# Optimization experiments

Hardware: AMD Instinct MI355X
Metric: run time of the kernel (lower is better)

## Reference

```python
import jax, jax.numpy as jnp
import numpy as np

FEAT_DIM = 128
GUIDE_DIM = 128
HIDDEN = [1024, 512, 256, 128]
OUT_DIM = 2


def make_coord(shape):
    # grid-center coords in (-1, 1), matching the torch make_coord
    seqs = [(-1.0 + 1.0 / n) + (2.0 / n) * jnp.arange(n, dtype=jnp.float32) for n in shape]
    yy, xx = jnp.meshgrid(seqs[0], seqs[1], indexing='ij')
    return jnp.stack([yy, xx], axis=-1)  # [h, w, 2]


def grid_sample_nearest(img, coord):
    # img: [B, C, H, W]; coord: [B, N, 2] with coord[...,0] along H, coord[...,1] along W
    # replicates F.grid_sample(img, coord.flip(-1)..., mode='nearest', align_corners=False,
    # padding_mode='zeros') followed by permute -> [B, N, C]
    B, C, H, W = img.shape
    iy = jnp.round(((coord[..., 0] + 1.0) * H - 1.0) * 0.5)
    ix = jnp.round(((coord[..., 1] + 1.0) * W - 1.0) * 0.5)
    valid = (iy >= 0) & (iy < H) & (ix >= 0) & (ix < W)
    iyc = jnp.clip(iy, 0, H - 1).astype(jnp.int32)
    ixc = jnp.clip(ix, 0, W - 1).astype(jnp.int32)
    g = jax.vmap(lambda im, y, x: im[:, y, x])(img, iyc, ixc)  # [B, C, N]
    g = g * valid[:, None, :].astype(img.dtype)  # zero padding outside
    return jnp.transpose(g, (0, 2, 1))  # [B, N, C]


def mlp(x, params):
    for W, b in params[:-1]:
        x = jax.nn.relu(x @ W + b)
    W, b = params[-1]
    return x @ W + b


def setup_inputs() -> dict:
    key = jax.random.key(0)
    ks = jax.random.split(key, 16)
    B, h, w = 4, 64, 64
    H_hr = W_hr = 256
    N = H_hr * W_hr  # 65536 query points
    feat = jax.random.normal(ks[0], (B, FEAT_DIM, h, w), jnp.float32)
    coord = jax.random.uniform(ks[1], (B, N, 2), jnp.float32, minval=-1.0, maxval=1.0)
    hr_guide = jax.random.normal(ks[2], (B, GUIDE_DIM, H_hr, W_hr), jnp.float32)
    lr_guide = jax.random.normal(ks[3], (B, GUIDE_DIM, h, w), jnp.float32)
    in_dim = FEAT_DIM + 2 * GUIDE_DIM + 2  # 386
    dims = [in_dim] + HIDDEN + [OUT_DIM]
    inp = {"feat": feat, "coord": coord, "hr_guide": hr_guide, "lr_guide": lr_guide}
    for i in range(len(dims) - 1):
        scale = 1.0 / np.sqrt(dims[i]).astype(np.float32)
        inp[f"W{i}"] = jax.random.normal(ks[4 + 2 * i], (dims[i], dims[i + 1]), jnp.float32) * scale
        inp[f"b{i}"] = jnp.zeros((dims[i + 1],), jnp.float32)
    return inp


def reference(feat, coord, hr_guide, lr_guide, W0, b0, W1, b1, W2, b2, W3, b3, W4, b4):
    params = [(W0, b0), (W1, b1), (W2, b2), (W3, b3), (W4, b4)]
    B, C, h, w = feat.shape
    N = coord.shape[1]
    fc = make_coord((h, w))  # [h, w, 2]
    feat_coord = jnp.broadcast_to(jnp.transpose(fc, (2, 0, 1))[None], (B, 2, h, w))
    q_guide_hr = grid_sample_nearest(hr_guide, coord)  # [B, N, G]
    rx = 1.0 / h
    ry = 1.0 / w
    hw = jnp.array([h, w], dtype=coord.dtype)
    preds = []
    for vx in (-1.0, 1.0):
        for vy in (-1.0, 1.0):
            shift = jnp.array([vx * rx, vy * ry], dtype=coord.dtype)
            coord_ = coord + shift
            q_feat = grid_sample_nearest(feat, coord_)        # [B, N, C]
            q_coord = grid_sample_nearest(feat_coord, coord_)  # [B, N, 2]
            rel_coord = (coord - q_coord) * hw                 # [B, N, 2]
            q_guide_lr = grid_sample_nearest(lr_guide, coord_)  # [B, N, G]
            inp = jnp.concatenate([q_feat, q_guide_hr, q_guide_hr - q_guide_lr, rel_coord], axis=-1)
            pred = mlp(inp.reshape(B * N, -1), params).reshape(B, N, OUT_DIM)
            preds.append(pred)
    preds = jnp.stack(preds, axis=-1)  # [B, N, 2, 4]
    weight = jax.nn.softmax(preds[:, :, 1, :], axis=-1)  # [B, N, 4]
    ret = jnp.sum(preds[:, :, 0, :] * weight, axis=-1, keepdims=True)  # [B, N, 1]
    return ret
```

## Files before the change

kernel.cpp:

```cpp
#include <hip/hip_runtime.h>
#include <cstdint>
#include <cstddef>


typedef unsigned short u16;
typedef unsigned int u32;
typedef _Float16 half8 __attribute__((ext_vector_type(8)));
typedef float floatx4 __attribute__((ext_vector_type(4)));
typedef u32 u32x2 __attribute__((ext_vector_type(2)));
typedef u32 u32x4 __attribute__((ext_vector_type(4)));

__device__ __forceinline__ u16 f2h(float x) {
    _Float16 h = (_Float16)x;
    return __builtin_bit_cast(unsigned short, h);
}
__device__ __forceinline__ float h2f(u16 u) {
    return (float)__builtin_bit_cast(_Float16, u);
}

__device__ __forceinline__ void cp_async16(const void* gsrc, void* lds) {
#if defined(__has_builtin) && __has_builtin(__builtin_amdgcn_global_load_lds)
    __builtin_amdgcn_global_load_lds(
        (__attribute__((address_space(1))) void*)(uintptr_t)gsrc,
        (__attribute__((address_space(3))) void*)(uint32_t)(uintptr_t)lds,
        16, 0, 0);
#else
    *(u32x4*)lds = *(const u32x4*)gsrc;
#endif
}

__global__ void transpose_chw_hwc(const float* __restrict__ src,
                                  u16* __restrict__ dst, int HW) {
    __shared__ float t[32][33];
    const int b = blockIdx.z;
    const int hw0 = blockIdx.x * 32, c0 = blockIdx.y * 32;
    const float* s = src + (size_t)b * 128 * HW;
    u16* d = dst + (size_t)b * HW * 128;
    const int tx = threadIdx.x, ty = threadIdx.y;
#pragma unroll
    for (int j = 0; j < 4; ++j)
        t[ty + j * 8][tx] = s[(size_t)(c0 + ty + j * 8) * HW + hw0 + tx];
    __syncthreads();
#pragma unroll
    for (int j = 0; j < 4; ++j)
        d[(size_t)(hw0 + ty + j * 8) * 128 + c0 + tx] = f2h(t[tx][ty + j * 8]);
}

__global__ void prep_wt(const float* __restrict__ W, u16* __restrict__ Wt,
                        int K, int N, int perm) {
    int idx = blockIdx.x * 256 + threadIdx.x;
    if (idx >= N * K) return;
    int nn = idx / K, kk = idx - nn * K;
    int ka = kk;
    if (perm) {
        int s = kk & 63;
        ka = (kk & ~63) + ((s & 3) << 4) + (s >> 2);
    }
    Wt[idx] = f2h(W[(size_t)ka * N + nn]);
}

__global__ __launch_bounds__(256) void gather_build(
    const float* __restrict__ coord, const u16* __restrict__ hrT,
    const u16* __restrict__ featT, const u16* __restrict__ lrT,
    u16* __restrict__ X, float* __restrict__ rel, int p0) {
    const int wid = threadIdx.x >> 6, lane = threadIdx.x & 63;
    const int pl = blockIdx.x * 4 + wid;
    const int p = p0 + pl;
    const int b = p >> 16;
    const float cy = coord[(size_t)p * 2];
    const float cx = coord[(size_t)p * 2 + 1];
    const u32* hr32 = (const u32*)hrT;
    const u32* ft32 = (const u32*)featT;
    const u32* lr32 = (const u32*)lrT;

    float fy = rintf(((cy + 1.0f) * 256.0f - 1.0f) * 0.5f);
    float fx = rintf(((cx + 1.0f) * 256.0f - 1.0f) * 0.5f);
    bool vh = (fy >= 0.0f) && (fy < 256.0f) && (fx >= 0.0f) && (fx < 256.0f);
    int iy = (int)fminf(fmaxf(fy, 0.0f), 255.0f);
    int ix = (int)fminf(fmaxf(fx, 0.0f), 255.0f);
    u32 hrv = hr32[((((size_t)b * 256 + iy) * 256 + ix) * 128 >> 1) + lane];
    if (!vh) hrv = 0u;
    const float hr_lo = h2f((u16)(hrv & 0xffffu));
    const float hr_hi = h2f((u16)(hrv >> 16));

    const size_t rowbase = (size_t)pl * 4;
#pragma unroll
    for (int s = 0; s < 4; ++s) {
        float sy = (s & 2) ? 0.015625f : -0.015625f;
        float sx = (s & 1) ? 0.015625f : -0.015625f;
        float gy = rintf(((cy + sy + 1.0f) * 64.0f - 1.0f) * 0.5f);
        float gx = rintf(((cx + sx + 1.0f) * 64.0f - 1.0f) * 0.5f);
        bool v = (gy >= 0.0f) && (gy < 64.0f) && (gx >= 0.0f) && (gx < 64.0f);
        int jy = (int)fminf(fmaxf(gy, 0.0f), 63.0f);
        int jx = (int)fminf(fmaxf(gx, 0.0f), 63.0f);
        size_t g32 = ((((size_t)b * 64 + jy) * 64 + jx) * 128 >> 1) + lane;
        u32 fv = ft32[g32];
        u32 lv = lr32[g32];
        if (!v) { fv = 0u; lv = 0u; }
        u16 d_lo = f2h(hr_lo - h2f((u16)(lv & 0xffffu)));
        u16 d_hi = f2h(hr_hi - h2f((u16)(lv >> 16)));

        u32* xr = (u32*)(X + (rowbase + s) * 384);
        xr[lane] = fv;
        xr[64 + lane] = hrv;
        xr[128 + lane] = (u32)d_lo | ((u32)d_hi << 16);

        if (lane == 0) {
            float qcy = v ? (-0.984375f + 0.03125f * (float)jy) : 0.0f;
            float qcx = v ? (-0.984375f + 0.03125f * (float)jx) : 0.0f;
            rel[(rowbase + s) * 2 + 0] = (cy - qcy) * 64.0f;
            rel[(rowbase + s) * 2 + 1] = (cx - qcx) * 64.0f;
        }
    }
}

__global__ __launch_bounds__(256, 3) void gemm_f16(
    const u16* __restrict__ A, const u16* __restrict__ Bt,
    const float* __restrict__ bias, u16* __restrict__ C, int K, int N,
    int lognb, const float* __restrict__ rel, const float* __restrict__ w0tail) {
    __shared__ __align__(16) u16 As[2][128 * 64];
    __shared__ __align__(16) u16 Bs[128 * 64];
    const int tid = threadIdx.x;
    const int lane = tid & 63;
    const int wid = tid >> 6;
    const int r = lane & 15, q = lane >> 4;
    const int wm = (wid & 1) << 6, wn = (wid >> 1) << 6;

    const int g = blockIdx.x;
    const int n_idx = (g >> 3) & ((1 << lognb) - 1);
    const int m_idx = (g & 7) + ((g >> (3 + lognb)) << 3);
    const int n0 = n_idx << 7;
    const u32 m0 = (u32)m_idx << 7;

    const int srow = tid >> 3;
    const int schunk = (tid & 7) ^ (srow & 7);
    const u32 gaoff = (m0 + (u32)srow) * (u32)K + ((u32)schunk << 3);
    const u32 gboff = (u32)(n0 + srow) * (u32)K + ((u32)schunk << 3);

    auto stageA = [&](int kt, int buf) {
        const u16* gak = A + gaoff + (kt << 6);
        u16* la = &As[buf][tid * 8];
#pragma unroll
        for (int i = 0; i < 4; ++i)
            cp_async16(gak + (u32)(i << 5) * (u32)K, la + (i << 11));
    };

    u32x4 breg[4];
    auto loadB = [&](int kt) {
        const u16* gbk = Bt + gboff + (kt << 6);
#pragma unroll
        for (int i = 0; i < 4; ++i)
            breg[i] = *(const u32x4*)(gbk + (u32)(i << 5) * (u32)K);
    };
    auto writeB = [&]() {
        u16* lb = &Bs[tid * 8];
#pragma unroll
        for (int i = 0; i < 4; ++i)
            *(u32x4*)(lb + (i << 11)) = breg[i];
    };

    const int cx = (q ^ (r & 7)) << 3;
    const int arow = (wm + r) << 6, brow = (wn + r) << 6;

    floatx4 acc[4][4];
#pragma unroll
    for (int mi = 0; mi < 4; ++mi)
#pragma unroll
        for (int ni = 0; ni < 4; ++ni)
            acc[mi][ni] = (floatx4){0.0f, 0.0f, 0.0f, 0.0f};

    const int nk = K >> 6;
    loadB(0);
    stageA(0, 0);
    writeB();
    __syncthreads();

    for (int kt = 0; kt < nk; ++kt) {
        const int cur = kt & 1;
        const bool pf = (kt + 1 < nk);
        if (pf) {
            loadB(kt + 1);
            stageA(kt + 1, cur ^ 1);
        }
#pragma unroll
        for (int ks = 0; ks < 2; ++ks) {
            half8 af[4], bf[4];
#pragma unroll
            for (int mi = 0; mi < 4; ++mi)
                af[mi] = *(const half8*)&As[cur][arow + (mi << 10) + (cx ^ (ks << 5))];
#pragma unroll
            for (int ni = 0; ni < 4; ++ni)
                bf[ni] = *(const half8*)&Bs[brow + (ni << 10) + (cx ^ (ks << 5))];
#pragma unroll
            for (int mi = 0; mi < 4; ++mi)
#pragma unroll
                for (int ni = 0; ni < 4; ++ni)
                    acc[mi][ni] = __builtin_amdgcn_mfma_f32_16x16x32_f16(
                        af[mi], bf[ni], acc[mi][ni], 0, 0, 0);
        }
        if (pf) {
            __syncthreads();
            writeB();
            __syncthreads();
        }
    }

    float bias_v[4], w0a[4], w0b[4];
#pragma unroll
    for (int ni = 0; ni < 4; ++ni) {
        int col = n0 + wn + ni * 16 + r;
        bias_v[ni] = bias[col];
        w0a[ni] = rel ? w0tail[col] : 0.0f;
        w0b[ni] = rel ? w0tail[N + col] : 0.0f;
    }
#pragma unroll
    for (int mi = 0; mi < 4; ++mi) {
#pragma unroll
        for (int rr = 0; rr < 4; ++rr) {
            u32 row = m0 + wm + mi * 16 + q * 4 + rr;
            float rl0 = 0.0f, rl1 = 0.0f;
            if (rel) {
                rl0 = rel[(size_t)row * 2];
                rl1 = rel[(size_t)row * 2 + 1];
            }
            u32 pk[2];
#pragma unroll
            for (int h = 0; h < 2; ++h) {
                u32 w = 0;
#pragma unroll
                for (int j = 0; j < 2; ++j) {
                    int ni = h * 2 + j;
                    float v = acc[mi][ni][rr] + bias_v[ni];
                    if (rel) v += rl0 * w0a[ni] + rl1 * w0b[ni];
                    v = fmaxf(v, 0.0f);
                    w |= (u32)f2h(v) << (16 * j);
                }
                pk[h] = w;
            }
            *(u32x2*)(C + row * (u32)N + (u32)(n0 + wn + (r << 2))) =
                (u32x2){pk[0], pk[1]};
        }
    }
}

__global__ __launch_bounds__(256) void l4_combine(
    const u16* __restrict__ A3, const float* __restrict__ W4,
    const float* __restrict__ b4, float* __restrict__ out, int p0) {
    const int wid = threadIdx.x >> 6, lane = threadIdx.x & 63;
    const int pl = blockIdx.x * 4 + wid;
    const int p2 = lane * 2;
    const int s0 = p2 & 63, bb = p2 & ~63;
    const int k0 = bb + ((s0 & 3) << 4) + (s0 >> 2);
    const int s1 = s0 + 1;
    const int k1 = bb + ((s1 & 3) << 4) + (s1 >> 2);
    const float w00 = W4[k0 * 2], w01 = W4[k0 * 2 + 1];
    const float w10 = W4[k1 * 2], w11 = W4[k1 * 2 + 1];
    float P0[4], P1[4];
#pragma unroll
    for (int s = 0; s < 4; ++s) {
        size_t rowoff = ((size_t)pl * 4 + s) * 128 + p2;
        u32 av = *(const u32*)(A3 + rowoff);
        float a0 = h2f((u16)(av & 0xffffu));
        float a1 = h2f((u16)(av >> 16));
        float d0 = a0 * w00 + a1 * w10;
        float d1 = a0 * w01 + a1 * w11;
#pragma unroll
        for (int m = 32; m >= 1; m >>= 1) {
            d0 += __shfl_xor(d0, m, 64);
            d1 += __shfl_xor(d1, m, 64);
        }
        P0[s] = d0 + b4[0];
        P1[s] = d1 + b4[1];
    }
    if (lane == 0) {
        float mx = fmaxf(fmaxf(P1[0], P1[1]), fmaxf(P1[2], P1[3]));
        float e0 = __expf(P1[0] - mx), e1 = __expf(P1[1] - mx);
        float e2 = __expf(P1[2] - mx), e3 = __expf(P1[3] - mx);
        float se = e0 + e1 + e2 + e3;
        out[p0 + pl] = (P0[0] * e0 + P0[1] * e1 + P0[2] * e2 + P0[3] * e3) / se;
    }
}

extern "C" void kernel_launch(void* const* d_in, const int* in_sizes, int n_in,
                              void* d_out, int out_size, void* d_ws,
                              size_t ws_size, hipStream_t stream) {
    const float* feat = (const float*)d_in[0];
    const float* coord = (const float*)d_in[1];
    const float* hr = (const float*)d_in[2];
    const float* lr = (const float*)d_in[3];
    const float* W0 = (const float*)d_in[4];
    const float* b0 = (const float*)d_in[5];
    const float* W1 = (const float*)d_in[6];
    const float* b1 = (const float*)d_in[7];
    const float* W2 = (const float*)d_in[8];
    const float* b2 = (const float*)d_in[9];
    const float* W3 = (const float*)d_in[10];
    const float* b3 = (const float*)d_in[11];
    const float* W4 = (const float*)d_in[12];
    const float* b4 = (const float*)d_in[13];
    float* out = (float*)d_out;

    char* base = (char*)d_ws;
    size_t off = 0;
    auto carve = [&](size_t bytes) -> char* {
        char* p = base + off;
        off += (bytes + 255) & ~(size_t)255;
        return p;
    };

    u16* hrT = (u16*)carve(4ull * 65536 * 128 * 2);
    u16* featT = (u16*)carve(4ull * 4096 * 128 * 2);
    u16* lrT = (u16*)carve(4ull * 4096 * 128 * 2);
    u16* Wt0 = (u16*)carve(1024ull * 384 * 2);
    u16* Wt1 = (u16*)carve(512ull * 1024 * 2);
    u16* Wt2 = (u16*)carve(256ull * 512 * 2);
    u16* Wt3 = (u16*)carve(128ull * 256 * 2);
    const size_t fixed = off;

    const size_t R = 1048576ull;
    int c = 1;
    for (; c < 8192; c *= 2) {
        size_t Rc = R / c;
        size_t need = fixed;
        size_t sizes[3] = {Rc * 1024, Rc * 8, Rc * 2048};
        for (int i = 0; i < 3; ++i) need += (sizes[i] + 255) & ~(size_t)255;
        if (need <= ws_size) break;
    }
    const size_t Rc = R / c;
    const int Pc = (int)(262144 / c);

    char* R1 = carve(Rc * 1024);
    float* rel = (float*)carve(Rc * 8);
    char* R2 = carve(Rc * 2048);
    u16* X = (u16*)R1;
    u16* A1 = (u16*)R1;
    u16* A0 = (u16*)R2;
    u16* A2 = (u16*)R2;
    u16* A3 = (u16*)(R2 + Rc * 512);

    transpose_chw_hwc<<<dim3(2048, 4, 4), dim3(32, 8), 0, stream>>>(hr, hrT, 65536);
    transpose_chw_hwc<<<dim3(128, 4, 4), dim3(32, 8), 0, stream>>>(feat, featT, 4096);
    transpose_chw_hwc<<<dim3(128, 4, 4), dim3(32, 8), 0, stream>>>(lr, lrT, 4096);
    prep_wt<<<(1024 * 384 + 255) / 256, 256, 0, stream>>>(W0, Wt0, 384, 1024, 0);
    prep_wt<<<(512 * 1024 + 255) / 256, 256, 0, stream>>>(W1, Wt1, 1024, 512, 1);
    prep_wt<<<(256 * 512 + 255) / 256, 256, 0, stream>>>(W2, Wt2, 512, 256, 1);
    prep_wt<<<(128 * 256 + 255) / 256, 256, 0, stream>>>(W3, Wt3, 256, 128, 1);

    const int mt = (int)(Rc / 128);
    for (int ci = 0; ci < c; ++ci) {
        const int p0 = ci * Pc;
        gather_build<<<Pc / 4, 256, 0, stream>>>(coord, hrT, featT, lrT, X, rel, p0);
        gemm_f16<<<mt * 8, 256, 0, stream>>>(X, Wt0, b0, A0, 384, 1024, 3, rel,
                                             W0 + 384 * 1024);
        gemm_f16<<<mt * 4, 256, 0, stream>>>(A0, Wt1, b1, A1, 1024, 512, 2,
                                             nullptr, nullptr);
        gemm_f16<<<mt * 2, 256, 0, stream>>>(A1, Wt2, b2, A2, 512, 256, 1,
                                             nullptr, nullptr);
        gemm_f16<<<mt * 1, 256, 0, stream>>>(A2, Wt3, b3, A3, 256, 128, 0,
                                             nullptr, nullptr);
        l4_combine<<<Pc / 4, 256, 0, stream>>>(A3, W4, b4, out, p0);
    }
}
```

Baseline: 3.971 ms.

## Add 256x256-tile 8-wave GEMM with LDS double buffering for the first three MLP layers

Adds a new fp16 MFMA GEMM kernel that uses 256x256 output tiles and 512 threads (8 waves, each computing 128x64). It stages A and B through double-buffered LDS with direct global-to-LDS loads, interleaves sub-tile loads with MFMA bursts under explicit waitcnt, barriers and setprio, and uses an XOR swizzle. The larger tiles raise arithmetic intensity and the interleaving is meant to hide load latency. The first three layers use it when the row count is a multiple of 2048, and the last layer keeps the old kernel. The trade-offs are heavier register and LDS use, fewer resident blocks, and fragile hand-written wait counts.

```diff
diff --git a/kernel.cpp b/kernel.cpp
--- a/kernel.cpp
+++ b/kernel.cpp
@@ -114,6 +114,179 @@
     }
 }
 
+__global__ __launch_bounds__(512, 2) void gemm_f16_256(
+    const u16* __restrict__ A, const u16* __restrict__ Bt,
+    const float* __restrict__ bias, u16* __restrict__ C, int K, int N,
+    int lognb, const float* __restrict__ rel, const float* __restrict__ w0tail) {
+    __shared__ __align__(16) u16 sA[2][2][8192];
+    __shared__ __align__(16) u16 sB[2][2][8192];
+    const int tid = threadIdx.x;
+    const int lane = tid & 63;
+    const int wid = tid >> 6;
+    const int r = lane & 15, q = lane >> 4;
+    const int wm = wid >> 2, wn = wid & 3;
+
+    const int g = blockIdx.x;
+    const int n_idx = (g >> 3) & ((1 << lognb) - 1);
+    const int m_idx = (g & 7) + ((g >> (3 + lognb)) << 3);
+    const int n0 = n_idx << 8;
+    const u32 m0 = (u32)m_idx << 8;
+
+    const u32 srow = (u32)(tid >> 2);
+    const u32 gchunk = (u32)((tid & 3) ^ ((tid >> 3) & 3));
+    const u32 gaoff = (m0 + srow) * (u32)K + (gchunk << 3);
+    const u32 gboff = ((u32)n0 + srow) * (u32)K + (gchunk << 3);
+
+    auto stageA = [&](int kt, int ks, int buf) {
+        const u16* gp = A + gaoff + (u32)((kt << 6) + (ks << 5));
+        u16* lp = &sA[buf][ks][tid << 3];
+        cp_async16(gp, lp);
+        cp_async16(gp + ((u32)K << 7), lp + 4096);
+    };
+    auto stageB = [&](int kt, int ks, int buf) {
+        const u16* gp = Bt + gboff + (u32)((kt << 6) + (ks << 5));
+        u16* lp = &sB[buf][ks][tid << 3];
+        cp_async16(gp, lp);
+        cp_async16(gp + ((u32)K << 7), lp + 4096);
+    };
+
+    const int fs = (q ^ ((r >> 1) & 3)) << 3;
+    const int abase = ((wm << 7) + r) * 32 + fs;
+    const int bbase = ((wn << 6) + r) * 32 + fs;
+
+    floatx4 acc[8][4];
+#pragma unroll
+    for (int mi = 0; mi < 8; ++mi)
+#pragma unroll
+        for (int ni = 0; ni < 4; ++ni)
+            acc[mi][ni] = (floatx4){0.0f, 0.0f, 0.0f, 0.0f};
+
+    const int nk = K >> 6;
+    stageA(0, 0, 0);
+    stageA(0, 1, 0);
+    stageB(0, 0, 0);
+    stageB(0, 1, 0);
+    const int k1 = (nk > 1) ? 1 : 0;
+    stageA(k1, 0, 1);
+    stageA(k1, 1, 1);
+    stageB(k1, 1, 1);
+    asm volatile("s_waitcnt vmcnt(6)");
+    __builtin_amdgcn_s_barrier();
+
+    for (int kt = 0; kt < nk; ++kt) {
+        const int cur = kt & 1, nxt = cur ^ 1;
+        const int ktp1 = (kt + 1 < nk) ? kt + 1 : nk - 1;
+        const int ktp2 = (kt + 2 < nk) ? kt + 2 : nk - 1;
+        half8 a0[8], a1[8], bf[2];
+#pragma unroll
+        for (int mi = 0; mi < 8; ++mi)
+            a0[mi] = *(const half8*)&sA[cur][0][abase + (mi << 9)];
+#pragma unroll
+        for (int ni = 0; ni < 2; ++ni)
+            bf[ni] = *(const half8*)&sB[cur][0][bbase + (ni << 9)];
+        stageB(ktp1, 0, nxt);
+        __builtin_amdgcn_s_barrier();
+        asm volatile("s_waitcnt lgkmcnt(0)");
+        __builtin_amdgcn_s_setprio(1);
+#pragma unroll
+        for (int mi = 0; mi < 8; ++mi)
+#pragma unroll
+            for (int ni = 0; ni < 2; ++ni)
+                acc[mi][ni] = __builtin_amdgcn_mfma_f32_16x16x32_f16(
+                    a0[mi], bf[ni], acc[mi][ni], 0, 0, 0);
+        __builtin_amdgcn_s_setprio(0);
+        __builtin_amdgcn_s_barrier();
+#pragma unroll
+        for (int mi = 0; mi < 8; ++mi)
+            a1[mi] = *(const half8*)&sA[cur][1][abase + (mi << 9)];
+#pragma unroll
+        for (int ni = 0; ni < 2; ++ni)
+            bf[ni] = *(const half8*)&sB[cur][1][bbase + (ni << 9)];
+        stageA(ktp2, 0, cur);
+        __builtin_amdgcn_s_barrier();
+        asm volatile("s_waitcnt lgkmcnt(0)");
+        __builtin_amdgcn_s_setprio(1);
+#pragma unroll
+        for (int mi = 0; mi < 8; ++mi)
+#pragma unroll
+            for (int ni = 0; ni < 2; ++ni)
+                acc[mi][ni] = __builtin_amdgcn_mfma_f32_16x16x32_f16(
+                    a1[mi], bf[ni], acc[mi][ni], 0, 0, 0);
+        __builtin_amdgcn_s_setprio(0);
+        __builtin_amdgcn_s_barrier();
+#pragma unroll
+        for (int ni = 0; ni < 2; ++ni)
+            bf[ni] = *(const half8*)&sB[cur][1][bbase + 1024 + (ni << 9)];
+        stageA(ktp2, 1, cur);
+        __builtin_amdgcn_s_barrier();
+        asm volatile("s_waitcnt lgkmcnt(0)");
+        __builtin_amdgcn_s_setprio(1);
+#pragma unroll
+        for (int mi = 0; mi < 8; ++mi)
+#pragma unroll
+            for (int ni = 0; ni < 2; ++ni)
+                acc[mi][2 + ni] = __builtin_amdgcn_mfma_f32_16x16x32_f16(
+                    a1[mi], bf[ni], acc[mi][2 + ni], 0, 0, 0);
+        __builtin_amdgcn_s_setprio(0);
+        __builtin_amdgcn_s_barrier();
+#pragma unroll
+        for (int ni = 0; ni < 2; ++ni)
+            bf[ni] = *(const half8*)&sB[cur][0][bbase + 1024 + (ni << 9)];
+        stageB(ktp2, 1, cur);
+        __builtin_amdgcn_s_barrier();
+        asm volatile("s_waitcnt lgkmcnt(0)");
+        __builtin_amdgcn_s_setprio(1);
+#pragma unroll
+        for (int mi = 0; mi < 8; ++mi)
+#pragma unroll
+            for (int ni = 0; ni < 2; ++ni)
+                acc[mi][2 + ni] = __builtin_amdgcn_mfma_f32_16x16x32_f16(
+                    a0[mi], bf[ni], acc[mi][2 + ni], 0, 0, 0);
+        __builtin_amdgcn_s_setprio(0);
+        asm volatile("s_waitcnt vmcnt(6)");
+        __builtin_amdgcn_s_barrier();
+    }
+    asm volatile("s_waitcnt vmcnt(0)");
+
+    float bias_v[4], w0a[4], w0b[4];
+#pragma unroll
+    for (int nig = 0; nig < 4; ++nig) {
+        int col = n0 + (wn << 6) + nig * 16 + r;
+        bias_v[nig] = bias[col];
+        w0a[nig] = rel ? w0tail[col] : 0.0f;
+        w0b[nig] = rel ? w0tail[N + col] : 0.0f;
+    }
+#pragma unroll
+    for (int mi = 0; mi < 8; ++mi) {
+#pragma unroll
+        for (int rr = 0; rr < 4; ++rr) {
+            u32 row = m0 + (u32)(wm << 7) + (u32)(mi << 4) + (u32)(q << 2) +
+                      (u32)rr;
+            float rl0 = 0.0f, rl1 = 0.0f;
+            if (rel) {
+                rl0 = rel[(size_t)row * 2];
+                rl1 = rel[(size_t)row * 2 + 1];
+            }
+            u32 pk[2];
+#pragma unroll
+            for (int h = 0; h < 2; ++h) {
+                u32 w = 0;
+#pragma unroll
+                for (int j = 0; j < 2; ++j) {
+                    int nig = h * 2 + j;
+                    float v = acc[mi][nig][rr] + bias_v[nig];
+                    if (rel) v += rl0 * w0a[nig] + rl1 * w0b[nig];
+                    v = fmaxf(v, 0.0f);
+                    w |= (u32)f2h(v) << (16 * j);
+                }
+                pk[h] = w;
+            }
+            *(u32x2*)(C + row * (u32)N + (u32)(n0 + (wn << 6) + (r << 2))) =
+                (u32x2){pk[0], pk[1]};
+        }
+    }
+}
+
 __global__ __launch_bounds__(256, 3) void gemm_f16(
     const u16* __restrict__ A, const u16* __restrict__ Bt,
     const float* __restrict__ bias, u16* __restrict__ C, int K, int N,
@@ -184,19 +357,19 @@
         }
 #pragma unroll
         for (int ks = 0; ks < 2; ++ks) {
-            half8 af[4], bf[4];
+            half8 af[4], bfr[4];
 #pragma unroll
             for (int mi = 0; mi < 4; ++mi)
                 af[mi] = *(const half8*)&As[cur][arow + (mi << 10) + (cx ^ (ks << 5))];
 #pragma unroll
             for (int ni = 0; ni < 4; ++ni)
-                bf[ni] = *(const half8*)&Bs[brow + (ni << 10) + (cx ^ (ks << 5))];
+                bfr[ni] = *(const half8*)&Bs[brow + (ni << 10) + (cx ^ (ks << 5))];
 #pragma unroll
             for (int mi = 0; mi < 4; ++mi)
 #pragma unroll
                 for (int ni = 0; ni < 4; ++ni)
                     acc[mi][ni] = __builtin_amdgcn_mfma_f32_16x16x32_f16(
-                        af[mi], bf[ni], acc[mi][ni], 0, 0, 0);
+                        af[mi], bfr[ni], acc[mi][ni], 0, 0, 0);
         }
         if (pf) {
             __syncthreads();
@@ -346,18 +519,29 @@
     prep_wt<<<(256 * 512 + 255) / 256, 256, 0, stream>>>(W2, Wt2, 512, 256, 1);
     prep_wt<<<(128 * 256 + 255) / 256, 256, 0, stream>>>(W3, Wt3, 256, 128, 1);
 
-    const int mt = (int)(Rc / 128);
+    const int mt1 = (int)(Rc / 128);
+    const int mt2 = (int)(Rc / 256);
+    const bool use256 = (Rc % 2048ull) == 0;
     for (int ci = 0; ci < c; ++ci) {
         const int p0 = ci * Pc;
         gather_build<<<Pc / 4, 256, 0, stream>>>(coord, hrT, featT, lrT, X, rel, p0);
-        gemm_f16<<<mt * 8, 256, 0, stream>>>(X, Wt0, b0, A0, 384, 1024, 3, rel,
-                                             W0 + 384 * 1024);
-        gemm_f16<<<mt * 4, 256, 0, stream>>>(A0, Wt1, b1, A1, 1024, 512, 2,
-                                             nullptr, nullptr);
-        gemm_f16<<<mt * 2, 256, 0, stream>>>(A1, Wt2, b2, A2, 512, 256, 1,
-                                             nullptr, nullptr);
-        gemm_f16<<<mt * 1, 256, 0, stream>>>(A2, Wt3, b3, A3, 256, 128, 0,
-                                             nullptr, nullptr);
+        if (use256) {
+            gemm_f16_256<<<mt2 * 4, 512, 0, stream>>>(X, Wt0, b0, A0, 384, 1024,
+                                                      2, rel, W0 + 384 * 1024);
+            gemm_f16_256<<<mt2 * 2, 512, 0, stream>>>(A0, Wt1, b1, A1, 1024, 512,
+                                                      1, nullptr, nullptr);
+            gemm_f16_256<<<mt2 * 1, 512, 0, stream>>>(A1, Wt2, b2, A2, 512, 256,
+                                                      0, nullptr, nullptr);
+        } else {
+            gemm_f16<<<mt1 * 8, 256, 0, stream>>>(X, Wt0, b0, A0, 384, 1024, 3,
+                                                  rel, W0 + 384 * 1024);
+            gemm_f16<<<mt1 * 4, 256, 0, stream>>>(A0, Wt1, b1, A1, 1024, 512, 2,
+                                                  nullptr, nullptr);
+            gemm_f16<<<mt1 * 2, 256, 0, stream>>>(A1, Wt2, b2, A2, 512, 256, 1,
+                                                  nullptr, nullptr);
+        }
+        gemm_f16<<<mt1 * 1, 256, 0, stream>>>(A2, Wt3, b3, A3, 256, 128, 0,
+                                              nullptr, nullptr);
         l4_combine<<<Pc / 4, 256, 0, stream>>>(A3, W4, b4, out, p0);
     }
 }
```

New measurement: 3.885 ms. -2.1%, faster.
